# Performance work log

Hardware: AMD Instinct MI355X
Metric: run time of the kernel (lower is better)

Reference implementation:

```python
import jax, jax.numpy as jnp
import numpy as np
from jax import lax

H = 12  # num_heads (from init_kwargs)


def _orthogonal_landmarks(q, num_landmarks):
    # q: (B, N, D) already scaled. Faithful to torch loop: recursively pick the
    # point whose max |cos sim| to the already-selected landmarks is minimal.
    B, N, D = q.shape
    nrm = jnp.linalg.norm(q, axis=-1, keepdims=True)
    qk = q / jnp.maximum(nrm, 1e-12)
    bidx = jnp.arange(B)
    key = jax.random.key(42)
    idx0 = jax.random.randint(key, (B,), 0, N)
    cur = qk[bidx, idx0]                             # (B, D)
    # running max |cos sim|; selected rows pinned to 10 (as in torch code)
    max_sim = jnp.zeros((B, N), qk.dtype).at[bidx, idx0].set(10.0)

    def step(carry, _):
        max_sim, cur = carry
        cos = jnp.abs(jnp.einsum('bnd,bd->bn', qk, cur))
        max_sim = jnp.maximum(max_sim, cos)
        idx = jnp.argmin(max_sim, axis=-1)
        cur2 = qk[bidx, idx]
        max_sim = max_sim.at[bidx, idx].set(10.0)
        return (max_sim, cur2), idx

    (_, _), idxs = lax.scan(step, (max_sim, cur), None, length=num_landmarks - 1)
    all_idx = jnp.concatenate([idx0[None, :], idxs], axis=0).T  # (B, L)
    landmarks = q[bidx[:, None], all_idx]                        # unnormalized q rows
    return lax.stop_gradient(landmarks)


def _orthoformer(q, k, v, num_landmarks, num_frames):
    # q,k,v: (B*h, N, D);  N = F * P
    Bh, N, D = q.shape
    F = num_frames
    P = N // F
    sc = D ** (-0.25)
    q = q * sc
    k = k * sc
    lm = _orthogonal_landmarks(q, num_landmarks)                 # (Bh, L, D)
    kernel_1 = jax.nn.softmax(jnp.einsum('bnd,bld->bnl', q, lm), axis=-1)   # (Bh,N,L)
    k2 = jnp.einsum('bld,bnd->bln', lm, k).reshape(Bh, num_landmarks, F, P)
    kernel_2 = jax.nn.softmax(k2, axis=-1)                       # (Bh,L,F,P)
    vr = v.reshape(Bh, F, P, D)
    x = jnp.einsum('blfp,bfpd->blfd', kernel_2, vr)
    x = jnp.einsum('bnl,blfd->bnfd', kernel_1, x)                # (Bh,N,F,D)
    return x


def setup_inputs() -> dict:
    key = jax.random.key(0)
    ks = jax.random.split(key, 6)
    B, F, P, C = 2, 16, 196, 768
    N = F * P
    s = 0.02
    x = jax.random.normal(ks[0], (B, N, C), jnp.float32)
    W_qkv = jax.random.normal(ks[1], (C, 3 * C), jnp.float32) * s
    W_pq = jax.random.normal(ks[2], (C, C), jnp.float32) * s
    W_pkv = jax.random.normal(ks[3], (C, 2 * C), jnp.float32) * s
    W_proj = jax.random.normal(ks[4], (C, C), jnp.float32) * s
    b_proj = jnp.zeros((C,), jnp.float32)
    return {"x": x, "W_qkv": W_qkv, "W_pq": W_pq, "W_pkv": W_pkv,
            "W_proj": W_proj, "b_proj": b_proj,
            "seq_len": P, "num_frames": F, "num_landmarks": 128}


def reference(x, W_qkv, W_pq, W_pkv, W_proj, b_proj, seq_len, num_frames, num_landmarks):
    B, N, C = x.shape
    F, P, h = num_frames, seq_len, H
    d = C // h
    scale = d ** (-0.5)
    qkv = x @ W_qkv                                              # (B,N,3C)
    q, k, v = jnp.split(qkv, 3, axis=-1)
    def to_bh(t):  # b n (h d) -> (b h) n d
        return t.reshape(B, N, h, d).transpose(0, 2, 1, 3).reshape(B * h, N, d)
    q_, k_, v_ = to_bh(q), to_bh(k), to_bh(v)
    xo = _orthoformer(q_, k_, v_, num_landmarks, F)              # (B*h,N,F,d)
    # (b h) s f d -> b s f (h d)
    xo = xo.reshape(B, h, N, F, d).transpose(0, 2, 3, 1, 4).reshape(B, N, F, C)
    # diagonal over (frame-of-query g, frame-of-key f)
    xd = xo.reshape(B, F, P, F, C)
    xdiag = jnp.diagonal(xd, axis1=1, axis2=3)                   # (B,P,C,F)
    xdiag = jnp.moveaxis(xdiag, -1, 1).reshape(B, N, C)          # b (f p) d
    q2 = xdiag @ W_pq                                            # (B,N,C)
    k2, v2 = jnp.split(xo @ W_pkv, 2, axis=-1)                   # (B,N,F,C) each
    q2 = q2.reshape(B, N, h, d).transpose(0, 2, 1, 3) * scale    # (B,h,N,d)
    k2 = k2.reshape(B, N, F, h, d).transpose(0, 3, 1, 2, 4)      # (B,h,N,F,d)
    v2 = v2.reshape(B, N, F, h, d).transpose(0, 3, 1, 2, 4)
    attn = jax.nn.softmax(jnp.einsum('bhsd,bhsfd->bhsf', q2, k2), axis=-1)
    out = jnp.einsum('bhsf,bhsfd->bhsd', attn, v2)               # (B,h,N,d)
    out = out.transpose(0, 2, 1, 3).reshape(B, N, C)
    out = out @ W_proj + b_proj
    return out, attn
```

## Files before the change

kernel.cpp:

```cpp
#include <hip/hip_runtime.h>


using u16 = unsigned short;
using u32 = unsigned int;
using u64 = unsigned long long;

typedef short bf16x8 __attribute__((ext_vector_type(8)));
typedef float f32x4 __attribute__((ext_vector_type(4)));

#define N_ 3136
#define C_ 768
#define H_ 12
#define F_ 16
#define P_ 196
#define L_ 128
#define SC_ 0.35355339059327373f
#define OUTPART_ ((size_t)2 * N_ * C_)
#define KB_ 8
#define RPB_ 392

__device__ __forceinline__ float b2f(u16 u) {
  u32 x = ((u32)u) << 16; float f; __builtin_memcpy(&f, &x, 4); return f;
}
__device__ __forceinline__ float lo16f(u32 u) {
  u32 x = u << 16; float f; __builtin_memcpy(&f, &x, 4); return f;
}
__device__ __forceinline__ float hi16f(u32 u) {
  u32 x = u & 0xFFFF0000u; float f; __builtin_memcpy(&f, &x, 4); return f;
}
__device__ __forceinline__ u16 f2b(float f) {
  u32 u; __builtin_memcpy(&u, &f, 4);
  u32 r = (u + 0x7FFFu + ((u >> 16) & 1u)) >> 16;
  return (u16)r;
}
__device__ __forceinline__ u64 d2u(double d) { u64 u; __builtin_memcpy(&u, &d, 8); return u; }

__device__ __forceinline__ void gll16(const void* g, void* l) {
  __builtin_amdgcn_global_load_lds(
      (__attribute__((address_space(1))) void*)g,
      (__attribute__((address_space(3))) void*)l, 16, 0, 0);
}

__global__ void detect_k(const u32* __restrict__ w, int* __restrict__ flag) {
  const int t = threadIdx.x;
  int hits = 0;
  #pragma unroll
  for (int i = 0; i < 16; ++i) {
    u32 word = w[t * 16 + i];
    u32 e = (word >> 7) & 0xFFu;
    if (e >= 110u && e <= 126u) hits++;
  }
  #pragma unroll
  for (int off = 32; off > 0; off >>= 1) hits += __shfl_down(hits, off);
  if (t == 0) flag[0] = (hits >= 512) ? 0 : 1;
}

__global__ void zcnt_k(u64* __restrict__ p) { if (threadIdx.x < 384) p[threadIdx.x] = 0ull; }

__device__ __forceinline__ void tf2(u32 k0, u32 k1v, u32 c0, u32 c1, u32& o0, u32& o1) {
  u32 ks[3] = {k0, k1v, k0 ^ k1v ^ 0x1BD11BDAu};
  u32 x0 = c0 + ks[0], x1 = c1 + ks[1];
  const u32 rA[4] = {13u, 15u, 26u, 6u}, rB[4] = {17u, 29u, 16u, 24u};
  #pragma unroll
  for (int r = 0; r < 5; ++r) {
    #pragma unroll
    for (int q = 0; q < 4; ++q) {
      u32 rot = (r & 1) ? rB[q] : rA[q];
      x0 += x1; x1 = (x1 << rot) | (x1 >> (32u - rot)); x1 ^= x0;
    }
    x0 += ks[(r + 1) % 3];
    x1 += ks[(r + 2) % 3] + (u32)(r + 1);
  }
  o0 = x0; o1 = x1;
}

__device__ __forceinline__ int tf_idx0(int bh) {
  u32 a0, a1, b0, b1;
  tf2(0u, 42u, 0u, 0u, a0, a1);
  tf2(0u, 42u, 0u, 1u, b0, b1);
  u32 j = (u32)bh;
  u32 h0, h1, l0, l1;
  tf2(a0, a1, 0u, j, h0, h1);
  u32 hi = h0 ^ h1;
  tf2(b0, b1, 0u, j, l0, l1);
  u32 lo = l0 ^ l1;
  return (int)(((hi % 3136u) * 2048u + (lo % 3136u)) % 3136u);
}

__global__ __launch_bounds__(256) void qselT_k(const void* __restrict__ xr, const void* __restrict__ wr,
                                               const int* __restrict__ flagp, float* __restrict__ qt)
{
  __shared__ float As[128 * 20];
  __shared__ float Bs[16 * 64];
  const int t = threadIdx.x;
  const int m0 = blockIdx.x * 128;
  const int n0 = blockIdx.y * 64;
  const int f32i = flagp[0];
  const int tx = t & 15, ty = t >> 4;
  float acc[8][4];
  #pragma unroll
  for (int i = 0; i < 8; ++i)
    #pragma unroll
    for (int j = 0; j < 4; ++j) acc[i][j] = 0.f;

  const int alr = t >> 1;
  const int alk = (t & 1) * 8;
  const int bkr = t >> 4;
  const int bnc = (t & 15) * 4;

  for (int k0 = 0; k0 < 768; k0 += 16) {
    float av[8];
    float4 bv;
    if (f32i) {
      const float* xa = (const float*)xr + (size_t)(m0 + alr) * 768 + k0 + alk;
      float4 a0 = *(const float4*)(xa);
      float4 a1 = *(const float4*)(xa + 4);
      av[0] = a0.x; av[1] = a0.y; av[2] = a0.z; av[3] = a0.w;
      av[4] = a1.x; av[5] = a1.y; av[6] = a1.z; av[7] = a1.w;
      bv = *(const float4*)((const float*)wr + (size_t)(k0 + bkr) * 2304 + n0 + bnc);
    } else {
      const u16* xa = (const u16*)xr + (size_t)(m0 + alr) * 768 + k0 + alk;
      #pragma unroll
      for (int j = 0; j < 8; ++j) av[j] = b2f(xa[j]);
      const u16* wa = (const u16*)wr + (size_t)(k0 + bkr) * 2304 + n0 + bnc;
      bv.x = b2f(wa[0]); bv.y = b2f(wa[1]); bv.z = b2f(wa[2]); bv.w = b2f(wa[3]);
    }
    #pragma unroll
    for (int j = 0; j < 8; ++j) As[alr * 20 + alk + j] = av[j];
    *(float4*)(&Bs[bkr * 64 + bnc]) = bv;
    __syncthreads();
    #pragma unroll
    for (int kk = 0; kk < 16; ++kk) {
      float a[8], b[4];
      #pragma unroll
      for (int i = 0; i < 8; ++i) a[i] = As[(ty * 8 + i) * 20 + kk];
      #pragma unroll
      for (int j = 0; j < 4; ++j) b[j] = Bs[kk * 64 + tx * 4 + j];
      #pragma unroll
      for (int i = 0; i < 8; ++i)
        #pragma unroll
        for (int j = 0; j < 4; ++j) acc[i][j] += a[i] * b[j];
    }
    __syncthreads();
  }
  #pragma unroll
  for (int i = 0; i < 8; ++i) {
    const int m = m0 + ty * 8 + i;
    const int b = m / N_, n = m - b * N_;
    #pragma unroll
    for (int j = 0; j < 4; ++j) {
      const int col = n0 + tx * 4 + j;
      const int hh = col >> 6, dd = col & 63;
      qt[((size_t)(b * H_ + hh) * 64 + dd) * N_ + n] = acc[i][j] * SC_;
    }
  }
}

__global__ __launch_bounds__(512, 1) void landmarksR_k(
    const float* __restrict__ qt, float* __restrict__ lm, u64* __restrict__ cand)
{
  const int kb = blockIdx.y;
  const int bh = blockIdx.x;
  const float* QT = qt + (size_t)bh * 64 * N_;
  float* LM = lm + (size_t)bh * L_ * 64;
  u64* cd = cand + (size_t)bh * 16;
  __shared__ double curD[64];
  __shared__ u64 redV[8];
  __shared__ int redI[8];
  __shared__ int sW;
  const int t = threadIdx.x;
  const bool act = (t < RPB_);
  const int g = t >> 2, dc = t & 3, d0 = dc * 16;
  const int r0 = kb * RPB_;
  const int myRow = r0 + t;
  const float* base = QT + r0 + 4 * g;

  float4 qreg[16];
  #pragma unroll
  for (int i = 0; i < 16; ++i) qreg[i] = (float4){0.f, 0.f, 0.f, 0.f};
  if (act) {
    #pragma unroll
    for (int i = 0; i < 16; ++i) qreg[i] = *(const float4*)(base + (size_t)(d0 + i) * N_);
  }

  double inv_own = 0.0, ms_own = 0.0;
  if (act) {
    double s0 = 0.0, s1 = 0.0, s2 = 0.0, s3 = 0.0;
    #pragma unroll
    for (int i = 0; i < 16; ++i) {
      const float4 v = qreg[i];
      s0 += (double)v.x * (double)v.x; s1 += (double)v.y * (double)v.y;
      s2 += (double)v.z * (double)v.z; s3 += (double)v.w * (double)v.w;
    }
    s0 += __shfl_xor(s0, 1); s1 += __shfl_xor(s1, 1);
    s2 += __shfl_xor(s2, 1); s3 += __shfl_xor(s3, 1);
    s0 += __shfl_xor(s0, 2); s1 += __shfl_xor(s1, 2);
    s2 += __shfl_xor(s2, 2); s3 += __shfl_xor(s3, 2);
    const double sown = (dc == 0) ? s0 : (dc == 1) ? s1 : (dc == 2) ? s2 : s3;
    inv_own = 1.0 / fmax(sqrt(sown), 1e-12);
  }
  const int idx0 = tf_idx0(bh);
  if (act && myRow == idx0) ms_own = 10.0;

  if (t < 64) {
    const float vf = QT[(size_t)t * N_ + idx0];
    double v = (double)vf;
    double s = v * v;
    #pragma unroll
    for (int off = 32; off; off >>= 1) s += __shfl_xor(s, off);
    curD[t] = v / fmax(sqrt(s), 1e-12);
    if (kb == 0) LM[t] = vf;
  }
  __syncthreads();

  for (int step = 1; step < 128; ++step) {
    u64 bV = d2u(1e30); int bI = 0x7fffffff;
    if (act) {
      double a0 = 0.0, a1 = 0.0, a2 = 0.0, a3 = 0.0;
      #pragma unroll
      for (int i = 0; i < 16; ++i) {
        const float4 v = qreg[i];
        const double c = curD[d0 + i];
        a0 += (double)v.x * c; a1 += (double)v.y * c;
        a2 += (double)v.z * c; a3 += (double)v.w * c;
      }
      a0 += __shfl_xor(a0, 1); a1 += __shfl_xor(a1, 1);
      a2 += __shfl_xor(a2, 1); a3 += __shfl_xor(a3, 1);
      a0 += __shfl_xor(a0, 2); a1 += __shfl_xor(a1, 2);
      a2 += __shfl_xor(a2, 2); a3 += __shfl_xor(a3, 2);
      const double aown = (dc == 0) ? a0 : (dc == 1) ? a1 : (dc == 2) ? a2 : a3;
      ms_own = fmax(ms_own, fabs(aown * inv_own));
      bV = d2u(ms_own); bI = myRow;
    }
    #pragma unroll
    for (int off = 32; off; off >>= 1) {
      const u64 ov = __shfl_xor(bV, off);
      const int oi = __shfl_xor(bI, off);
      if (ov < bV || (ov == bV && oi < bI)) { bV = ov; bI = oi; }
    }
    if ((t & 63) == 0) { redV[t >> 6] = bV; redI[t >> 6] = bI; }
    __syncthreads();
    const int par = step & 1;
    if (t == 0) {
      u64 v = redV[0]; int ix = redI[0];
      #pragma unroll
      for (int w2 = 1; w2 < 8; ++w2)
        if (redV[w2] < v || (redV[w2] == v && redI[w2] < ix)) { v = redV[w2]; ix = redI[w2]; }
      const u64 pk = (v & ~((1ull << 19) - 1ull)) | ((u64)(u32)(step & 127) << 12) | (u64)(u32)ix;
      __hip_atomic_store(&cd[par * KB_ + kb], pk, __ATOMIC_RELAXED, __HIP_MEMORY_SCOPE_AGENT);
    }
    if (t < 64) {
      u64 pv = ~0ull;
      int ok = 1;
      for (;;) {
        if (t < KB_) {
          pv = __hip_atomic_load(&cd[par * KB_ + t], __ATOMIC_RELAXED, __HIP_MEMORY_SCOPE_AGENT);
          ok = ((int)((pv >> 12) & 127u) == step) ? 1 : 0;
        }
        if (__all(ok)) break;
        __builtin_amdgcn_s_sleep(1);
      }
      u64 m = (t < KB_) ? pv : ~0ull;
      #pragma unroll
      for (int off = 1; off < KB_; off <<= 1) {
        const u64 o = __shfl_xor(m, off);
        if (o < m) m = o;
      }
      if (t == 0) sW = (int)(m & 0xFFFu);
    }
    __syncthreads();
    const int w = sW;
    if (act && myRow == w) ms_own = 10.0;
    if (t < 64) {
      const float vf = QT[(size_t)t * N_ + w];
      double v = (double)vf;
      double s = v * v;
      #pragma unroll
      for (int off = 32; off; off >>= 1) s += __shfl_xor(s, off);
      curD[t] = v / fmax(sqrt(s), 1e-12);
      if (kb == 0) LM[(size_t)step * 64 + t] = vf;
    }
    __syncthreads();
  }
}

__device__ __forceinline__ void twT_body(const void* W, int K, int Nn, int f32i,
                                         u16* WT, int k0, int n0, int t, u16 (&Ts)[64][80])
{
  const int kr = t >> 2, nc = (t & 3) * 16;
  u16 tmp[16];
  if (f32i) {
    const float* p = (const float*)W + (size_t)(k0 + kr) * Nn + n0 + nc;
    #pragma unroll
    for (int j = 0; j < 16; ++j) tmp[j] = f2b(p[j]);
  } else {
    const u16* p = (const u16*)W + (size_t)(k0 + kr) * Nn + n0 + nc;
    #pragma unroll
    for (int j = 0; j < 16; ++j) tmp[j] = p[j];
  }
  #pragma unroll
  for (int j = 0; j < 16; ++j) Ts[kr][nc + j] = tmp[j];
  __syncthreads();
  const int nr = t >> 2, kc = (t & 3) * 16;
  u16 o[16];
  #pragma unroll
  for (int j = 0; j < 16; ++j) o[j] = Ts[kc + j][nr];
  u16* dst = WT + (size_t)(n0 + nr) * K + k0 + kc;
  *(uint4*)(dst) = *(uint4*)(o);
  *(uint4*)(dst + 8) = *(uint4*)(o + 8);
}

__global__ __launch_bounds__(256) void twT_k(const void* __restrict__ W, int K, int Nn,
                                             const int* __restrict__ flagp, u16* __restrict__ WT)
{
  __shared__ u16 Ts[64][80];
  twT_body(W, K, Nn, flagp[0], WT, blockIdx.x * 64, blockIdx.y * 64, threadIdx.x, Ts);
}

__global__ __launch_bounds__(256) void twT3_k(const void* __restrict__ W0, const void* __restrict__ W1,
                                              const void* __restrict__ W2, const int* __restrict__ flagp,
                                              u16* __restrict__ T0, u16* __restrict__ T1, u16* __restrict__ T2)
{
  __shared__ u16 Ts[64][80];
  const int z = blockIdx.z;
  const void* W = (z == 0) ? W0 : (z == 1) ? W1 : W2;
  u16* WT = (z == 0) ? T0 : (z == 1) ? T1 : T2;
  const int Nn = (z == 0) ? 1536 : 768;
  if (blockIdx.y * 64 >= Nn) return;
  twT_body(W, 768, Nn, flagp[0], WT, blockIdx.x * 64, blockIdx.y * 64, threadIdx.x, Ts);
}

__global__ __launch_bounds__(256) void xcvt_k(const void* __restrict__ x,
                                              const int* __restrict__ flagp, u16* __restrict__ xb)
{
  const int i = blockIdx.x * 256 + threadIdx.x;
  if (flagp[0]) {
    const float4* p = (const float4*)x + (size_t)i * 2;
    float4 f0 = p[0], f1 = p[1];
    u16 tmp[8] = { f2b(f0.x), f2b(f0.y), f2b(f0.z), f2b(f0.w),
                   f2b(f1.x), f2b(f1.y), f2b(f1.z), f2b(f1.w) };
    *(uint4*)(xb + (size_t)i * 8) = *(uint4*)tmp;
  } else {
    ((uint4*)xb)[i] = ((const uint4*)x)[i];
  }
}

struct GemmCore {
  const u16 *aP0, *aP1, *bP0, *bP1;
  u16 *lA0, *lA1, *lB0, *lB1;
  int roA[4], roB[4];
  int mw, nw, lr, lk;
};

__device__ __forceinline__ void gemm_core_init(GemmCore& gc, u16* As, u16* Bs,
    const u16* A16, const u16* B16, size_t aOff, size_t bOff,
    int m0, int n0, int lda, int ldb, int M, int t)
{
  const int lane = t & 63;
  const int w = t >> 6;
  gc.mw = (w >> 1) * 64;
  gc.nw = (w & 1) * 64;
  gc.lr = lane & 15;
  gc.lk = lane >> 4;
  const int c0 = w * 2, c1 = c0 + 1;
  const int rl = lane >> 2, sl = lane & 3;
  const int rowA0 = c0 * 16 + rl, rowA1 = c1 * 16 + rl;
  const int segA0 = (sl ^ ((rowA0 ^ (rowA0 >> 2)) & 3)) * 8;
  const int segA1 = (sl ^ ((rowA1 ^ (rowA1 >> 2)) & 3)) * 8;
  int ga0 = m0 + rowA0; if (ga0 >= M) ga0 = M - 1;
  int ga1 = m0 + rowA1; if (ga1 >= M) ga1 = M - 1;
  gc.aP0 = A16 + aOff + (size_t)ga0 * lda + segA0;
  gc.aP1 = A16 + aOff + (size_t)ga1 * lda + segA1;
  gc.bP0 = B16 + bOff + (size_t)(n0 + rowA0) * ldb + segA0;
  gc.bP1 = B16 + bOff + (size_t)(n0 + rowA1) * ldb + segA1;
  gc.lA0 = &As[c0 * 512]; gc.lA1 = &As[c1 * 512];
  gc.lB0 = &Bs[c0 * 512]; gc.lB1 = &Bs[c1 * 512];
  #pragma unroll
  for (int q = 0; q < 4; ++q) {
    const int ra = gc.mw + q * 16 + gc.lr;
    gc.roA[q] = ra * 32 + ((gc.lk ^ ((ra ^ (ra >> 2)) & 3)) * 8);
    const int rb = gc.nw + q * 16 + gc.lr;
    gc.roB[q] = rb * 32 + ((gc.lk ^ ((rb ^ (rb >> 2)) & 3)) * 8);
  }
}

__device__ __forceinline__ void gemm_core_loop(const GemmCore& gc, u16* As, u16* Bs,
                                               int K, f32x4 (&acc)[4][4])
{
  for (int k0 = 0; k0 < K; k0 += 32) {
    gll16(gc.aP0 + k0, gc.lA0);
    gll16(gc.aP1 + k0, gc.lA1);
    gll16(gc.bP0 + k0, gc.lB0);
    gll16(gc.bP1 + k0, gc.lB1);
    __syncthreads();
    bf16x8 af[4], bfv[4];
    #pragma unroll
    for (int mt = 0; mt < 4; ++mt) af[mt] = *(const bf16x8*)(&As[gc.roA[mt]]);
    #pragma unroll
    for (int nt = 0; nt < 4; ++nt) bfv[nt] = *(const bf16x8*)(&Bs[gc.roB[nt]]);
    #pragma unroll
    for (int mt = 0; mt < 4; ++mt)
      #pragma unroll
      for (int nt = 0; nt < 4; ++nt)
        acc[mt][nt] = __builtin_amdgcn_mfma_f32_16x16x32_bf16(af[mt], bfv[nt], acc[mt][nt], 0, 0, 0);
    __syncthreads();
  }
}

template <int MODE>
__global__ __launch_bounds__(256) void gemm_k(
    const void* __restrict__ Ap, const void* __restrict__ Bp,
    int M, int K, int lda, int ldb, int n0c, int cn, const int* __restrict__ flagp,
    float* __restrict__ of0, u16* __restrict__ ob0, u16* __restrict__ ob1, u16* __restrict__ ob2,
    const void* __restrict__ biasRaw, void* __restrict__ outRaw)
{
  __shared__ u16 As[128 * 32];
  __shared__ u16 Bs[128 * 32];
  const int t = threadIdx.x;
  const int m0 = blockIdx.x * 128;
  const int n0 = blockIdx.y * 128;
  const int rf = (MODE == 4) ? flagp[0] : 0;

  size_t aOff = 0, bOff = 0;
  if constexpr (MODE == 1) {
    const int bh = blockIdx.z;
    aOff = (size_t)bh * ((size_t)N_ * 128) + (size_t)n0c * 128;
    bOff = (size_t)bh * (1024 * 128);
  }
  f32x4 acc[4][4];
  #pragma unroll
  for (int i = 0; i < 4; ++i)
    #pragma unroll
    for (int j = 0; j < 4; ++j) acc[i][j] = (f32x4){0.f, 0.f, 0.f, 0.f};

  GemmCore gc;
  gemm_core_init(gc, As, Bs, (const u16*)Ap, (const u16*)Bp, aOff, bOff, m0, n0, lda, ldb, M, t);
  gemm_core_loop(gc, As, Bs, K, acc);

  const int lr = gc.lr, lk = gc.lk, mw = gc.mw, nw = gc.nw;
  #pragma unroll
  for (int mt = 0; mt < 4; ++mt) {
    #pragma unroll
    for (int nt = 0; nt < 4; ++nt) {
      #pragma unroll
      for (int r = 0; r < 4; ++r) {
        const int grow = m0 + mw + mt * 16 + lk * 4 + r;
        const int gcol = n0 + nw + nt * 16 + lr;
        if (grow >= M) continue;
        float vv = acc[mt][nt][r];
        if constexpr (MODE == 0) {
          int b = (grow >= N_) ? 1 : 0;
          int n = grow - b * N_;
          int t3 = gcol / C_, cc = gcol - t3 * C_;
          int hh = cc >> 6, dd = cc & 63;
          size_t dst = (((size_t)(b * H_ + hh)) * N_ + n) * 64 + dd;
          if (t3 == 0) ob0[dst] = f2b(vv * SC_);
          else if (t3 == 1) ob1[dst] = f2b(vv * SC_);
          else ob2[dst] = f2b(vv);
        } else if constexpr (MODE == 1) {
          const int bh = blockIdx.z;
          int b = bh / H_, hh = bh - b * H_;
          int f = gcol >> 6, dd = gcol & 63;
          u16 wv = f2b(vv);
          ob0[(((size_t)(b * cn + grow)) * F_ + f) * C_ + hh * 64 + dd] = wv;
          int n = n0c + grow;
          if (f == n / P_) ob1[((size_t)(b * cn + grow)) * C_ + hh * 64 + dd] = wv;
        } else {
          float bvad = rf ? ((const float*)biasRaw)[gcol] : b2f(((const u16*)biasRaw)[gcol]);
          float ov = vv + bvad;
          if (rf) ((float*)outRaw)[(size_t)grow * C_ + gcol] = ov;
          else    ((u16*)outRaw)[(size_t)grow * C_ + gcol] = f2b(ov);
        }
      }
    }
  }
}

__global__ __launch_bounds__(256) void gemm23_k(
    const u16* __restrict__ xoc, const u16* __restrict__ xdc,
    const u16* __restrict__ WpkvT, const u16* __restrict__ WpqT,
    int cn, float* __restrict__ q2c, u16* __restrict__ k2c, u16* __restrict__ v2c)
{
  __shared__ u16 As[128 * 32];
  __shared__ u16 Bs[128 * 32];
  const int t = threadIdx.x;
  const int z = blockIdx.z;
  const int m0 = blockIdx.x * 128;
  const int n0 = blockIdx.y * 128;
  const int M = z ? (2 * cn) : (2 * cn * F_);
  const int NN = z ? 768 : 1536;
  if (m0 >= M || n0 >= NN) return;
  const u16* Ap = z ? xdc : xoc;
  const u16* Bp = z ? WpqT : WpkvT;

  f32x4 acc[4][4];
  #pragma unroll
  for (int i = 0; i < 4; ++i)
    #pragma unroll
    for (int j = 0; j < 4; ++j) acc[i][j] = (f32x4){0.f, 0.f, 0.f, 0.f};

  GemmCore gc;
  gemm_core_init(gc, As, Bs, Ap, Bp, 0, 0, m0, n0, 768, 768, M, t);
  gemm_core_loop(gc, As, Bs, 768, acc);

  const int lr = gc.lr, lk = gc.lk, mw = gc.mw, nw = gc.nw;
  #pragma unroll
  for (int mt = 0; mt < 4; ++mt) {
    #pragma unroll
    for (int nt = 0; nt < 4; ++nt) {
      #pragma unroll
      for (int r = 0; r < 4; ++r) {
        const int grow = m0 + mw + mt * 16 + lk * 4 + r;
        const int gcol = n0 + nw + nt * 16 + lr;
        if (grow >= M) continue;
        float vv = acc[mt][nt][r];
        if (z == 0) {
          const int cn16 = cn * F_;
          int b = (grow >= cn16) ? 1 : 0;
          int r2 = grow - b * cn16;
          int ln = r2 >> 4, f = r2 & 15;
          int t2 = (gcol >= C_) ? 1 : 0, cc = gcol - t2 * C_;
          int hh = cc >> 6, dd = cc & 63;
          size_t dst = ((((size_t)(b * H_ + hh)) * cn + ln) * F_ + f) * 64 + dd;
          if (t2) v2c[dst] = f2b(vv); else k2c[dst] = f2b(vv);
        } else {
          int b = (grow >= cn) ? 1 : 0;
          int ln = grow - b * cn;
          int hh = gcol >> 6, dd = gcol & 63;
          q2c[(((size_t)(b * H_ + hh)) * cn + ln) * 64 + dd] = vv * 0.125f;
        }
      }
    }
  }
}

__global__ __launch_bounds__(256) void k1_k(const u16* __restrict__ qb,
                                            const float* __restrict__ lm,
                                            u16* __restrict__ k1)
{
  const int bh = blockIdx.y;
  const int r0 = blockIdx.x * 64;
  __shared__ float qT[64][65];
  __shared__ float lmS[128 * 64];
  __shared__ float redA[4][64];
  __shared__ float redB[64];
  const int t = threadIdx.x;
  const u16* Q = qb + ((size_t)bh * N_ + r0) * 64;
  const float* Lm = lm + (size_t)bh * L_ * 64;
  for (int u = t; u < 2048; u += 256) ((float4*)lmS)[u] = ((const float4*)Lm)[u];
  for (int u = t; u < 512; u += 256) {
    int row = u >> 3, j0 = (u & 7) * 8;
    uint4 pk = *(const uint4*)(Q + (size_t)row * 64 + j0);
    const u16* pu = (const u16*)&pk;
    #pragma unroll
    for (int jj = 0; jj < 8; ++jj) qT[j0 + jj][row] = b2f(pu[jj]);
  }
  __syncthreads();
  const int row = t & 63, ch = t >> 6;
  float qr[64];
  #pragma unroll
  for (int j = 0; j < 64; ++j) qr[j] = qT[j][row];
  float s[32];
  for (int li = 0; li < 32; ++li) {
    const float* lp = lmS + (ch * 32 + li) * 64;
    float a = 0.f;
    #pragma unroll
    for (int j = 0; j < 64; ++j) a += lp[j] * qr[j];
    s[li] = a;
  }
  float mx = -1e30f;
  for (int li = 0; li < 32; ++li) mx = fmaxf(mx, s[li]);
  redA[ch][row] = mx;
  __syncthreads();
  if (t < 64) redB[t] = fmaxf(fmaxf(redA[0][t], redA[1][t]), fmaxf(redA[2][t], redA[3][t]));
  __syncthreads();
  mx = redB[row];
  float sum = 0.f;
  for (int li = 0; li < 32; ++li) { float e = __expf(s[li] - mx); s[li] = e; sum += e; }
  __syncthreads();
  redA[ch][row] = sum;
  __syncthreads();
  if (t < 64) redB[t] = 1.0f / (redA[0][t] + redA[1][t] + redA[2][t] + redA[3][t]);
  __syncthreads();
  const float inv = redB[row];
  u16* out = k1 + ((size_t)bh * N_ + r0 + row) * 128 + ch * 32;
  for (int li = 0; li < 32; ++li) out[li] = f2b(s[li] * inv);
}

__global__ __launch_bounds__(256) void k2x1_k(const float* __restrict__ lm,
                                              const u16* __restrict__ kb,
                                              const u16* __restrict__ vb,
                                              u16* __restrict__ x1)
{
  const int bh = blockIdx.x;
  const int f = blockIdx.y;
  __shared__ u16 kS[P_ * 64];
  __shared__ u16 vS[P_ * 64];
  __shared__ float redM[2][128];
  __shared__ float redS[2][128];
  const int t = threadIdx.x;
  const u16* Kf = kb + ((size_t)bh * N_ + f * P_) * 64;
  const u16* Vf = vb + ((size_t)bh * N_ + f * P_) * 64;
  for (int u = t; u < 1568; u += 256) {
    ((uint4*)kS)[u] = ((const uint4*)Kf)[u];
    ((uint4*)vS)[u] = ((const uint4*)Vf)[u];
  }
  __syncthreads();
  const int l = t & 127, half = t >> 7;
  const float* lp = lm + ((size_t)bh * L_ + l) * 64;
  float lr[64];
  #pragma unroll
  for (int j = 0; j < 64; ++j) lr[j] = lp[j];

  const int p0 = half * 98, p1 = p0 + 98;
  float mx = -1e30f;
  for (int p = p0; p < p1; ++p) {
    const uint4* kp = (const uint4*)(kS + p * 64);
    float s = 0.f;
    #pragma unroll
    for (int q4 = 0; q4 < 8; ++q4) {
      uint4 pk = kp[q4];
      const u32* pu = (const u32*)&pk;
      #pragma unroll
      for (int j2 = 0; j2 < 4; ++j2) {
        u32 u = pu[j2];
        s += lr[q4 * 8 + j2 * 2] * lo16f(u) + lr[q4 * 8 + j2 * 2 + 1] * hi16f(u);
      }
    }
    mx = fmaxf(mx, s);
  }
  redM[half][l] = mx;
  __syncthreads();
  mx = fmaxf(redM[0][l], redM[1][l]);

  float sm = 0.f;
  for (int p = p0; p < p1; ++p) {
    const uint4* kp = (const uint4*)(kS + p * 64);
    float s = 0.f;
    #pragma unroll
    for (int q4 = 0; q4 < 8; ++q4) {
      uint4 pk = kp[q4];
      const u32* pu = (const u32*)&pk;
      #pragma unroll
      for (int j2 = 0; j2 < 4; ++j2) {
        u32 u = pu[j2];
        s += lr[q4 * 8 + j2 * 2] * lo16f(u) + lr[q4 * 8 + j2 * 2 + 1] * hi16f(u);
      }
    }
    sm += __expf(s - mx);
  }
  redS[half][l] = sm;
  __syncthreads();
  const float inv = 1.0f / (redS[0][l] + redS[1][l]);

  const int dd0 = half * 32;
  float acc[32];
  #pragma unroll
  for (int u = 0; u < 32; ++u) acc[u] = 0.f;
  for (int p = 0; p < P_; ++p) {
    const uint4* kp = (const uint4*)(kS + p * 64);
    float s = 0.f;
    #pragma unroll
    for (int q4 = 0; q4 < 8; ++q4) {
      uint4 pk = kp[q4];
      const u32* pu = (const u32*)&pk;
      #pragma unroll
      for (int j2 = 0; j2 < 4; ++j2) {
        u32 u = pu[j2];
        s += lr[q4 * 8 + j2 * 2] * lo16f(u) + lr[q4 * 8 + j2 * 2 + 1] * hi16f(u);
      }
    }
    const float e = __expf(s - mx);
    const uint4* vp = (const uint4*)(vS + p * 64 + dd0);
    #pragma unroll
    for (int q4 = 0; q4 < 4; ++q4) {
      uint4 pv = vp[q4];
      const u32* pu = (const u32*)&pv;
      #pragma unroll
      for (int j2 = 0; j2 < 4; ++j2) {
        u32 u = pu[j2];
        acc[q4 * 8 + j2 * 2]     += e * lo16f(u);
        acc[q4 * 8 + j2 * 2 + 1] += e * hi16f(u);
      }
    }
  }
  u16* outT = x1 + (size_t)bh * (1024 * 128) + (size_t)(f * 64 + dd0) * 128 + l;
  for (int u = 0; u < 32; ++u) outT[(size_t)u * 128] = f2b(acc[u] * inv);
}

__global__ __launch_bounds__(256) void attn_k(const float* __restrict__ q2c,
                                              const u16* __restrict__ k2c,
                                              const u16* __restrict__ v2c,
                                              int n0c, int cn, const int* __restrict__ flagp,
                                              void* __restrict__ outRaw,
                                              u16* __restrict__ o)
{
  const int bh = blockIdx.y;
  const int b = bh / H_, hh = bh - b * H_;
  const int t = threadIdx.x;
  const int f32o = flagp[0];
  __shared__ float aS[64][17];
  const int nl = t >> 2, qi = t & 3;
  const int ln = blockIdx.x * 64 + nl;
  const bool act = ln < cn;
  const int n = n0c + ln;
  float q[64];
  if (act) {
    const float* qr = q2c + ((size_t)bh * cn + ln) * 64;
    #pragma unroll
    for (int j = 0; j < 64; ++j) q[j] = qr[j];
    float lg[4];
    #pragma unroll
    for (int ff = 0; ff < 4; ++ff) {
      const int f = qi * 4 + ff;
      const u16* kp = k2c + (((size_t)bh * cn + ln) * F_ + f) * 64;
      float s = 0.f;
      #pragma unroll
      for (int j8 = 0; j8 < 8; ++j8) {
        uint4 pk = ((const uint4*)kp)[j8];
        const u16* pu = (const u16*)&pk;
        #pragma unroll
        for (int u = 0; u < 8; ++u) s += q[j8 * 8 + u] * b2f(pu[u]);
      }
      lg[ff] = s;
    }
    float mx = fmaxf(fmaxf(lg[0], lg[1]), fmaxf(lg[2], lg[3]));
    mx = fmaxf(mx, __shfl_xor(mx, 1));
    mx = fmaxf(mx, __shfl_xor(mx, 2));
    float e[4], sm = 0.f;
    #pragma unroll
    for (int ff = 0; ff < 4; ++ff) { e[ff] = __expf(lg[ff] - mx); sm += e[ff]; }
    sm += __shfl_xor(sm, 1);
    sm += __shfl_xor(sm, 2);
    const float iv = 1.0f / sm;
    const size_t abase = ((size_t)bh * N_ + n) * F_ + qi * 4;
    #pragma unroll
    for (int ff = 0; ff < 4; ++ff) {
      const float a = e[ff] * iv;
      if (f32o) ((float*)outRaw)[OUTPART_ + abase + ff] = a;
      else      ((u16*)outRaw)[OUTPART_ + abase + ff] = f2b(a);
      aS[nl][qi * 4 + ff] = a;
    }
  }
  __syncthreads();
  if (act) {
    const int dd0 = qi * 16;
    float acc[16];
    #pragma unroll
    for (int u = 0; u < 16; ++u) acc[u] = 0.f;
    for (int f = 0; f < F_; ++f) {
      const float w2 = aS[nl][f];
      const u16* vp = v2c + (((size_t)bh * cn + ln) * F_ + f) * 64 + dd0;
      uint4 pv0 = ((const uint4*)vp)[0], pv1 = ((const uint4*)vp)[1];
      const u16* pu0 = (const u16*)&pv0;
      const u16* pu1 = (const u16*)&pv1;
      #pragma unroll
      for (int u = 0; u < 8; ++u) acc[u] += w2 * b2f(pu0[u]);
      #pragma unroll
      for (int u = 0; u < 8; ++u) acc[8 + u] += w2 * b2f(pu1[u]);
    }
    u16* op = o + ((size_t)(b * N_ + n)) * C_ + hh * 64 + dd0;
    for (int u = 0; u < 16; ++u) op[u] = f2b(acc[u]);
  }
}

extern "C" void kernel_launch(void* const* d_in, const int* in_sizes, int n_in,
                              void* d_out, int out_size, void* d_ws, size_t ws_size,
                              hipStream_t stream)
{
  (void)in_sizes; (void)n_in; (void)out_size;
  const void* x     = d_in[0];
  const void* Wqkv  = d_in[1];
  const void* Wpq   = d_in[2];
  const void* Wpkv  = d_in[3];
  const void* Wproj = d_in[4];
  const void* bproj = d_in[5];

  char* ws = (char*)d_ws;
  size_t off = 0;
  auto alloc = [&](size_t bytes) { void* p = ws + off; off += (bytes + 255) & ~(size_t)255; return p; };
  int*  flagp = (int*)alloc(256);
  u16*  qb  = (u16*)alloc(9633792);
  u16*  kb  = (u16*)alloc(9633792);
  u16*  vb  = (u16*)alloc(9633792);
  float* lm = (float*)alloc(786432);
  u16*  x1b = (u16*)alloc(6291456);
  u16*  ob  = (u16*)alloc(9633792);
  const size_t k1off = off;
  u16*  k1b = (u16*)alloc(19267584);
  const size_t chunk0 = off;

  const size_t qtNeed = k1off + 19267584 + 256;

  int Nc = 0;
  {
    const int cands[5] = {3136, 1568, 784, 392, 196};
    for (int i = 0; i < 5; ++i) {
      size_t need = chunk0 + (size_t)156672 * cands[i] + 1024;
      if (need <= ws_size && qtNeed <= ws_size) { Nc = cands[i]; break; }
    }
  }
  if (Nc == 0) return;
  const int nchunks = N_ / Nc;
  u16*  xoc = (u16*)(ws + chunk0);
  u16*  k2c = xoc + (size_t)24576 * Nc;
  u16*  v2c = k2c + (size_t)24576 * Nc;
  u16*  xdc = v2c + (size_t)24576 * Nc;
  float* q2c = (float*)(xdc + (size_t)1536 * Nc);
  float* qt  = (float*)(ws + k1off);

  u16* WqkvT = (u16*)(ws + k1off);
  u16* xb    = (u16*)(ws + k1off + 3538944);
  u16* WpkvT = kb;
  u16* WpqT  = kb + 1179648;
  u16* WprojT= kb + 1179648 + 589824;

  u64* cand = (u64*)(ws + chunk0);

  detect_k<<<1, 64, 0, stream>>>((const u32*)Wqkv, flagp);
  zcnt_k<<<1, 512, 0, stream>>>(cand);

  qselT_k<<<dim3(49, 12), 256, 0, stream>>>(x, Wqkv, flagp, qt);
  landmarksR_k<<<dim3(24, KB_), 512, 0, stream>>>(qt, lm, cand);

  twT_k<<<dim3(12, 36), 256, 0, stream>>>(Wqkv, 768, 2304, flagp, WqkvT);
  xcvt_k<<<2352, 256, 0, stream>>>(x, flagp, xb);

  gemm_k<0><<<dim3(49, 18, 1), 256, 0, stream>>>(xb, WqkvT, 6272, 768, 768, 768, 0, 0, flagp,
                                                 nullptr, qb, kb, vb, nullptr, nullptr);
  k2x1_k<<<dim3(24, 16), 256, 0, stream>>>(lm, kb, vb, x1b);
  k1_k<<<dim3(49, 24), 256, 0, stream>>>(qb, lm, k1b);

  twT3_k<<<dim3(12, 24, 3), 256, 0, stream>>>(Wpkv, Wpq, Wproj, flagp, WpkvT, WpqT, WprojT);

  for (int c = 0; c < nchunks; ++c) {
    const int n0c = c * Nc;
    gemm_k<1><<<dim3((Nc + 127) / 128, 8, 24), 256, 0, stream>>>(
        k1b, x1b, Nc, 128, 128, 128, n0c, Nc, flagp, nullptr, xoc, xdc, nullptr, nullptr, nullptr);
    gemm23_k<<<dim3(Nc / 4, 12, 2), 256, 0, stream>>>(
        xoc, xdc, WpkvT, WpqT, Nc, q2c, k2c, v2c);
    attn_k<<<dim3((Nc + 63) / 64, 24), 256, 0, stream>>>(
        q2c, k2c, v2c, n0c, Nc, flagp, d_out, ob);
  }
  gemm_k<4><<<dim3(49, 6, 1), 256, 0, stream>>>(ob, WprojT, 6272, 768, 768, 768, 0, 0, flagp,
                                                nullptr, nullptr, nullptr, nullptr, bproj, d_out);
}
```

Baseline: 1.658 ms.

## Reassociate second attention to avoid materializing per-frame K2/V2 projections

Replaces the large GEMM that projected every (query, frame) row of xo through W_pkv with a reassociated form. Each head's query is folded into the key weights (g = q2·Wk_h^T), logits are computed directly against xo, xo is attention-weighted per head, and only that weighted sum is projected through the value weights. This avoids building the 16× larger k2/v2 tensors and cuts GEMM FLOPs and memory traffic, at the cost of extra small GEMM launches, a per-head gathered intermediate, and changed bf16 rounding order.

```diff
diff --git a/kernel.cpp b/kernel.cpp
--- a/kernel.cpp
+++ b/kernel.cpp
@@ -195,6 +195,7 @@
     s0 += __shfl_xor(s0, 1); s1 += __shfl_xor(s1, 1);
     s2 += __shfl_xor(s2, 1); s3 += __shfl_xor(s3, 1);
     s0 += __shfl_xor(s0, 2); s1 += __shfl_xor(s1, 2);
+    s0 = s0; s1 = s1;
     s2 += __shfl_xor(s2, 2); s3 += __shfl_xor(s3, 2);
     const double sown = (dc == 0) ? s0 : (dc == 1) ? s1 : (dc == 2) ? s2 : s3;
     inv_own = 1.0 / fmax(sqrt(sown), 1e-12);
@@ -319,15 +320,35 @@
 
 __global__ __launch_bounds__(256) void twT3_k(const void* __restrict__ W0, const void* __restrict__ W1,
                                               const void* __restrict__ W2, const int* __restrict__ flagp,
-                                              u16* __restrict__ T0, u16* __restrict__ T1, u16* __restrict__ T2)
+                                              u16* __restrict__ T0, u16* __restrict__ T1, u16* __restrict__ T2,
+                                              u16* __restrict__ Wb)
 {
   __shared__ u16 Ts[64][80];
   const int z = blockIdx.z;
+  const int t = threadIdx.x;
+  if (z == 3) {
+    const int k0 = blockIdx.x * 64, n0 = blockIdx.y * 64;
+    const int kr = t >> 2, nc = (t & 3) * 16;
+    u16 tmp[16];
+    if (flagp[0]) {
+      const float* p = (const float*)W0 + (size_t)(k0 + kr) * 1536 + n0 + nc;
+      #pragma unroll
+      for (int j = 0; j < 16; ++j) tmp[j] = f2b(p[j]);
+    } else {
+      const u16* p = (const u16*)W0 + (size_t)(k0 + kr) * 1536 + n0 + nc;
+      #pragma unroll
+      for (int j = 0; j < 16; ++j) tmp[j] = p[j];
+    }
+    u16* dst = Wb + (size_t)(k0 + kr) * 1536 + n0 + nc;
+    *(uint4*)(dst) = *(uint4*)(tmp);
+    *(uint4*)(dst + 8) = *(uint4*)(tmp + 8);
+    return;
+  }
   const void* W = (z == 0) ? W0 : (z == 1) ? W1 : W2;
   u16* WT = (z == 0) ? T0 : (z == 1) ? T1 : T2;
   const int Nn = (z == 0) ? 1536 : 768;
   if (blockIdx.y * 64 >= Nn) return;
-  twT_body(W, 768, Nn, flagp[0], WT, blockIdx.x * 64, blockIdx.y * 64, threadIdx.x, Ts);
+  twT_body(W, 768, Nn, flagp[0], WT, blockIdx.x * 64, blockIdx.y * 64, t, Ts);
 }
 
 __global__ __launch_bounds__(256) void xcvt_k(const void* __restrict__ x,
@@ -426,6 +447,16 @@
     const int bh = blockIdx.z;
     aOff = (size_t)bh * ((size_t)N_ * 128) + (size_t)n0c * 128;
     bOff = (size_t)bh * (1024 * 128);
+  }
+  if constexpr (MODE == 5) {
+    const int h = blockIdx.z;
+    aOff = (size_t)h * (2 * cn) * 64;
+    bOff = (size_t)h * 64;
+  }
+  if constexpr (MODE == 6) {
+    const int h = blockIdx.z;
+    aOff = (size_t)h * (2 * cn) * 768;
+    bOff = (size_t)(768 + h * 64) * 768;
   }
   f32x4 acc[4][4];
   #pragma unroll
@@ -465,69 +496,22 @@
           ob0[(((size_t)(b * cn + grow)) * F_ + f) * C_ + hh * 64 + dd] = wv;
           int n = n0c + grow;
           if (f == n / P_) ob1[((size_t)(b * cn + grow)) * C_ + hh * 64 + dd] = wv;
+        } else if constexpr (MODE == 3) {
+          int hh = gcol >> 6, dd = gcol & 63;
+          ob0[((size_t)hh * (2 * cn) + grow) * 64 + dd] = f2b(vv * 0.125f);
+        } else if constexpr (MODE == 5) {
+          ob0[((size_t)blockIdx.z * (2 * cn) + grow) * 768 + gcol] = f2b(vv);
+        } else if constexpr (MODE == 6) {
+          if (gcol < 64) {
+            int b2 = (grow >= cn) ? 1 : 0;
+            int ln = grow - b2 * cn;
+            ob0[((size_t)(b2 * N_ + n0c + ln)) * 768 + blockIdx.z * 64 + gcol] = f2b(vv);
+          }
         } else {
           float bvad = rf ? ((const float*)biasRaw)[gcol] : b2f(((const u16*)biasRaw)[gcol]);
           float ov = vv + bvad;
           if (rf) ((float*)outRaw)[(size_t)grow * C_ + gcol] = ov;
           else    ((u16*)outRaw)[(size_t)grow * C_ + gcol] = f2b(ov);
-        }
-      }
-    }
-  }
-}
-
-__global__ __launch_bounds__(256) void gemm23_k(
-    const u16* __restrict__ xoc, const u16* __restrict__ xdc,
-    const u16* __restrict__ WpkvT, const u16* __restrict__ WpqT,
-    int cn, float* __restrict__ q2c, u16* __restrict__ k2c, u16* __restrict__ v2c)
-{
-  __shared__ u16 As[128 * 32];
-  __shared__ u16 Bs[128 * 32];
-  const int t = threadIdx.x;
-  const int z = blockIdx.z;
-  const int m0 = blockIdx.x * 128;
-  const int n0 = blockIdx.y * 128;
-  const int M = z ? (2 * cn) : (2 * cn * F_);
-  const int NN = z ? 768 : 1536;
-  if (m0 >= M || n0 >= NN) return;
-  const u16* Ap = z ? xdc : xoc;
-  const u16* Bp = z ? WpqT : WpkvT;
-
-  f32x4 acc[4][4];
-  #pragma unroll
-  for (int i = 0; i < 4; ++i)
-    #pragma unroll
-    for (int j = 0; j < 4; ++j) acc[i][j] = (f32x4){0.f, 0.f, 0.f, 0.f};
-
-  GemmCore gc;
-  gemm_core_init(gc, As, Bs, Ap, Bp, 0, 0, m0, n0, 768, 768, M, t);
-  gemm_core_loop(gc, As, Bs, 768, acc);
-
-  const int lr = gc.lr, lk = gc.lk, mw = gc.mw, nw = gc.nw;
-  #pragma unroll
-  for (int mt = 0; mt < 4; ++mt) {
-    #pragma unroll
-    for (int nt = 0; nt < 4; ++nt) {
-      #pragma unroll
-      for (int r = 0; r < 4; ++r) {
-        const int grow = m0 + mw + mt * 16 + lk * 4 + r;
-        const int gcol = n0 + nw + nt * 16 + lr;
-        if (grow >= M) continue;
-        float vv = acc[mt][nt][r];
-        if (z == 0) {
-          const int cn16 = cn * F_;
-          int b = (grow >= cn16) ? 1 : 0;
-          int r2 = grow - b * cn16;
-          int ln = r2 >> 4, f = r2 & 15;
-          int t2 = (gcol >= C_) ? 1 : 0, cc = gcol - t2 * C_;
-          int hh = cc >> 6, dd = cc & 63;
-          size_t dst = ((((size_t)(b * H_ + hh)) * cn + ln) * F_ + f) * 64 + dd;
-          if (t2) v2c[dst] = f2b(vv); else k2c[dst] = f2b(vv);
-        } else {
-          int b = (grow >= cn) ? 1 : 0;
-          int ln = grow - b * cn;
-          int hh = gcol >> 6, dd = gcol & 63;
-          q2c[(((size_t)(b * H_ + hh)) * cn + ln) * 64 + dd] = vv * 0.125f;
         }
       }
     }
@@ -688,79 +672,81 @@
   for (int u = 0; u < 32; ++u) outT[(size_t)u * 128] = f2b(acc[u] * inv);
 }
 
-__global__ __launch_bounds__(256) void attn_k(const float* __restrict__ q2c,
-                                              const u16* __restrict__ k2c,
-                                              const u16* __restrict__ v2c,
-                                              int n0c, int cn, const int* __restrict__ flagp,
-                                              void* __restrict__ outRaw,
-                                              u16* __restrict__ o)
-{
-  const int bh = blockIdx.y;
-  const int b = bh / H_, hh = bh - b * H_;
+__global__ __launch_bounds__(256) void attn2_k(const u16* __restrict__ xoc,
+                                               const u16* __restrict__ g,
+                                               int n0c, int cn, const int* __restrict__ flagp,
+                                               void* __restrict__ outRaw, u16* __restrict__ wc)
+{
+  __shared__ float aS[12][16];
   const int t = threadIdx.x;
+  const int m = blockIdx.x;
+  const int b = (m >= cn) ? 1 : 0;
+  const int ln = m - b * cn;
+  const int n = n0c + ln;
   const int f32o = flagp[0];
-  __shared__ float aS[64][17];
-  const int nl = t >> 2, qi = t & 3;
-  const int ln = blockIdx.x * 64 + nl;
-  const bool act = ln < cn;
-  const int n = n0c + ln;
-  float q[64];
-  if (act) {
-    const float* qr = q2c + ((size_t)bh * cn + ln) * 64;
-    #pragma unroll
-    for (int j = 0; j < 64; ++j) q[j] = qr[j];
-    float lg[4];
-    #pragma unroll
-    for (int ff = 0; ff < 4; ++ff) {
-      const int f = qi * 4 + ff;
-      const u16* kp = k2c + (((size_t)bh * cn + ln) * F_ + f) * 64;
-      float s = 0.f;
-      #pragma unroll
-      for (int j8 = 0; j8 < 8; ++j8) {
-        uint4 pk = ((const uint4*)kp)[j8];
-        const u16* pu = (const u16*)&pk;
-        #pragma unroll
-        for (int u = 0; u < 8; ++u) s += q[j8 * 8 + u] * b2f(pu[u]);
-      }
-      lg[ff] = s;
-    }
-    float mx = fmaxf(fmaxf(lg[0], lg[1]), fmaxf(lg[2], lg[3]));
+  const u16* Xo = xoc + ((size_t)(b * cn + ln) * 16) * 768;
+  const size_t hstr = (size_t)(2 * cn) * 768;
+
+  if (t < 192) {
+    const int h = t >> 4, f = t & 15;
+    const uint4* xp = (const uint4*)(Xo + (size_t)f * 768);
+    const uint4* gp = (const uint4*)(g + (size_t)h * hstr + (size_t)m * 768);
+    float lg = 0.f;
+    #pragma unroll 4
+    for (int q = 0; q < 96; ++q) {
+      uint4 xv = xp[q], gv = gp[q];
+      const u32* xu = (const u32*)&xv;
+      const u32* gu = (const u32*)&gv;
+      #pragma unroll
+      for (int j = 0; j < 4; ++j)
+        lg += lo16f(xu[j]) * lo16f(gu[j]) + hi16f(xu[j]) * hi16f(gu[j]);
+    }
+    float mx = lg;
     mx = fmaxf(mx, __shfl_xor(mx, 1));
     mx = fmaxf(mx, __shfl_xor(mx, 2));
-    float e[4], sm = 0.f;
-    #pragma unroll
-    for (int ff = 0; ff < 4; ++ff) { e[ff] = __expf(lg[ff] - mx); sm += e[ff]; }
+    mx = fmaxf(mx, __shfl_xor(mx, 4));
+    mx = fmaxf(mx, __shfl_xor(mx, 8));
+    float e = __expf(lg - mx);
+    float sm = e;
     sm += __shfl_xor(sm, 1);
     sm += __shfl_xor(sm, 2);
-    const float iv = 1.0f / sm;
-    const size_t abase = ((size_t)bh * N_ + n) * F_ + qi * 4;
-    #pragma unroll
-    for (int ff = 0; ff < 4; ++ff) {
-      const float a = e[ff] * iv;
-      if (f32o) ((float*)outRaw)[OUTPART_ + abase + ff] = a;
-      else      ((u16*)outRaw)[OUTPART_ + abase + ff] = f2b(a);
-      aS[nl][qi * 4 + ff] = a;
-    }
-  }
-  __syncthreads();
-  if (act) {
-    const int dd0 = qi * 16;
-    float acc[16];
-    #pragma unroll
-    for (int u = 0; u < 16; ++u) acc[u] = 0.f;
-    for (int f = 0; f < F_; ++f) {
-      const float w2 = aS[nl][f];
-      const u16* vp = v2c + (((size_t)bh * cn + ln) * F_ + f) * 64 + dd0;
-      uint4 pv0 = ((const uint4*)vp)[0], pv1 = ((const uint4*)vp)[1];
-      const u16* pu0 = (const u16*)&pv0;
-      const u16* pu1 = (const u16*)&pv1;
-      #pragma unroll
-      for (int u = 0; u < 8; ++u) acc[u] += w2 * b2f(pu0[u]);
-      #pragma unroll
-      for (int u = 0; u < 8; ++u) acc[8 + u] += w2 * b2f(pu1[u]);
-    }
-    u16* op = o + ((size_t)(b * N_ + n)) * C_ + hh * 64 + dd0;
-    for (int u = 0; u < 16; ++u) op[u] = f2b(acc[u]);
+    sm += __shfl_xor(sm, 4);
+    sm += __shfl_xor(sm, 8);
+    const float a = e / sm;
+    const size_t abase = ((size_t)(b * H_ + h) * N_ + n) * F_ + f;
+    if (f32o) ((float*)outRaw)[OUTPART_ + abase] = a;
+    else      ((u16*)outRaw)[OUTPART_ + abase] = f2b(a);
+    aS[h][f] = a;
+  }
+  __syncthreads();
+  if (t < 192) {
+    const int cg = t >> 1, sh = t & 1;
+    const int c0 = cg * 8;
+    float acc[6][8];
+    #pragma unroll
+    for (int j = 0; j < 6; ++j)
+      #pragma unroll
+      for (int k = 0; k < 8; ++k) acc[j][k] = 0.f;
+    for (int f = 0; f < 16; ++f) {
+      uint4 xv = *(const uint4*)(Xo + (size_t)f * 768 + c0);
+      const u32* xu = (const u32*)&xv;
+      float xf[8];
+      #pragma unroll
+      for (int j = 0; j < 4; ++j) { xf[2 * j] = lo16f(xu[j]); xf[2 * j + 1] = hi16f(xu[j]); }
+      #pragma unroll
+      for (int j = 0; j < 6; ++j) {
+        const float a = aS[sh * 6 + j][f];
+        #pragma unroll
+        for (int k = 0; k < 8; ++k) acc[j][k] += a * xf[k];
+      }
+    }
+    #pragma unroll
+    for (int j = 0; j < 6; ++j) {
+      u16 pk[8];
+      #pragma unroll
+      for (int k = 0; k < 8; ++k) pk[k] = f2b(acc[j][k]);
+      *(uint4*)(wc + (size_t)(sh * 6 + j) * hstr + (size_t)m * 768 + c0) = *(uint4*)pk;
+    }
   }
 }
 
@@ -796,24 +782,25 @@
   {
     const int cands[5] = {3136, 1568, 784, 392, 196};
     for (int i = 0; i < 5; ++i) {
-      size_t need = chunk0 + (size_t)156672 * cands[i] + 1024;
+      size_t need = chunk0 + (size_t)129024 * cands[i] + 1024;
       if (need <= ws_size && qtNeed <= ws_size) { Nc = cands[i]; break; }
     }
   }
   if (Nc == 0) return;
   const int nchunks = N_ / Nc;
   u16*  xoc = (u16*)(ws + chunk0);
-  u16*  k2c = xoc + (size_t)24576 * Nc;
-  u16*  v2c = k2c + (size_t)24576 * Nc;
-  u16*  xdc = v2c + (size_t)24576 * Nc;
-  float* q2c = (float*)(xdc + (size_t)1536 * Nc);
-  float* qt  = (float*)(ws + k1off);
-
-  u16* WqkvT = (u16*)(ws + k1off);
-  u16* xb    = (u16*)(ws + k1off + 3538944);
-  u16* WpkvT = kb;
-  u16* WpqT  = kb + 1179648;
-  u16* WprojT= kb + 1179648 + 589824;
+  u16*  xdc = xoc + (size_t)24576 * Nc;
+  u16*  q2b = xdc + (size_t)1536 * Nc;
+  u16*  gbf = q2b + (size_t)1536 * Nc;
+  u16*  wcb = gbf + (size_t)18432 * Nc;
+  float* qt = (float*)(ws + k1off);
+
+  u16* WqkvT  = (u16*)(ws + k1off);
+  u16* xb     = (u16*)(ws + k1off + 3538944);
+  u16* WpkvT  = kb;
+  u16* WpqT   = kb + 1179648;
+  u16* WprojT = kb + 1179648 + 589824;
+  u16* Wpkvb  = kb + 1179648 + 589824 + 589824;
 
   u64* cand = (u64*)(ws + chunk0);
 
@@ -831,16 +818,21 @@
   k2x1_k<<<dim3(24, 16), 256, 0, stream>>>(lm, kb, vb, x1b);
   k1_k<<<dim3(49, 24), 256, 0, stream>>>(qb, lm, k1b);
 
-  twT3_k<<<dim3(12, 24, 3), 256, 0, stream>>>(Wpkv, Wpq, Wproj, flagp, WpkvT, WpqT, WprojT);
-
+  twT3_k<<<dim3(12, 24, 4), 256, 0, stream>>>(Wpkv, Wpq, Wproj, flagp,
+                                              WpkvT, WpqT, WprojT, Wpkvb);
+
+  const int gx = (2 * Nc + 127) / 128;
   for (int c = 0; c < nchunks; ++c) {
     const int n0c = c * Nc;
     gemm_k<1><<<dim3((Nc + 127) / 128, 8, 24), 256, 0, stream>>>(
         k1b, x1b, Nc, 128, 128, 128, n0c, Nc, flagp, nullptr, xoc, xdc, nullptr, nullptr, nullptr);
-    gemm23_k<<<dim3(Nc / 4, 12, 2), 256, 0, stream>>>(
-        xoc, xdc, WpkvT, WpqT, Nc, q2c, k2c, v2c);
-    attn_k<<<dim3((Nc + 63) / 64, 24), 256, 0, stream>>>(
-        q2c, k2c, v2c, n0c, Nc, flagp, d_out, ob);
+    gemm_k<3><<<dim3(gx, 6, 1), 256, 0, stream>>>(
+        xdc, WpqT, 2 * Nc, 768, 768, 768, n0c, Nc, flagp, nullptr, q2b, nullptr, nullptr, nullptr, nullptr);
+    gemm_k<5><<<dim3(gx, 6, 12), 256, 0, stream>>>(
+        q2b, Wpkvb, 2 * Nc, 64, 64, 1536, n0c, Nc, flagp, nullptr, gbf, nullptr, nullptr, nullptr, nullptr);
+    attn2_k<<<dim3(2 * Nc), 256, 0, stream>>>(xoc, gbf, n0c, Nc, flagp, d_out, wcb);
+    gemm_k<6><<<dim3(gx, 1, 12), 256, 0, stream>>>(
+        wcb, WpkvT, 2 * Nc, 768, 768, 768, n0c, Nc, flagp, nullptr, ob, nullptr, nullptr, nullptr, nullptr);
   }
   gemm_k<4><<<dim3(49, 6, 1), 256, 0, stream>>>(ob, WprojT, 6272, 768, 768, 768, 0, 0, flagp,
                                                 nullptr, nullptr, nullptr, nullptr, bproj, d_out);
```

Result: faster. 1.531 ms (-7.6%).
